# Kernel tuning notes

Hardware: AMD Instinct MI355X
Metric: run time of the kernel (lower is better)

## Reference

```python
import jax, jax.numpy as jnp
import numpy as np

B, S1, T = 32, 128, 50
E, H, L, V = 768, 1024, 3, 32000


def setup_inputs() -> dict:
    key = jax.random.key(0)
    ks = jax.random.split(key, 32)
    s = 0.02
    inp = {
        "x": jax.random.normal(ks[0], (B, S1, E), jnp.float32),
        "target_seq": jax.random.randint(ks[1], (B, T), 0, V),
        "emb": jax.random.normal(ks[2], (V, E), jnp.float32) * s,
        "attn_W1": jax.random.normal(ks[3], (H, E + H), jnp.float32) * s,
        "attn_b1": jnp.zeros((H,), jnp.float32),
        "attn_W2": jax.random.normal(ks[4], (1, H), jnp.float32) * s,
        "attn_b2": jnp.zeros((1,), jnp.float32),
        "fc_W": jax.random.normal(ks[5], (V, H), jnp.float32) * s,
        "fc_b": jnp.zeros((V,), jnp.float32),
    }
    for l in range(L):
        in_dim = 2 * E if l == 0 else H
        inp[f"Wih{l}"] = jax.random.normal(ks[6 + 4 * l], (4 * H, in_dim), jnp.float32) * s
        inp[f"Whh{l}"] = jax.random.normal(ks[7 + 4 * l], (4 * H, H), jnp.float32) * s
        inp[f"bih{l}"] = jnp.zeros((4 * H,), jnp.float32)
        inp[f"bhh{l}"] = jnp.zeros((4 * H,), jnp.float32)
    return inp


def _forward(x, target_seq, emb, attn_W1, attn_b1, attn_W2, attn_b2,
             Wih0, Whh0, bih0, bhh0, Wih1, Whh1, bih1, bhh1,
             Wih2, Whh2, bih2, bhh2, fc_W, fc_b):
    Bb, S, Edim = x.shape
    Hd = Whh0.shape[1]
    W1x, W1h = attn_W1[:, :Edim], attn_W1[:, Edim:]
    # precompute encoder-side part of the additive attention MLP: (B, S, H)
    xW = jnp.einsum('bse,he->bsh', x, W1x)
    emb_in = emb[target_seq]  # teacher forcing inputs (B, T, E)
    Wihs = (Wih0, Wih1, Wih2)
    Whhs = (Whh0, Whh1, Whh2)
    bihs = (bih0, bih1, bih2)
    bhhs = (bhh0, bhh1, bhh2)

    def step(carry, cur_in):
        h, c = carry  # each (L, B, H)
        hid = jax.nn.relu(xW + (h[-1] @ W1h.T)[:, None, :] + attn_b1)  # (B,S,H)
        scores = hid @ attn_W2[0] + attn_b2[0]  # (B, S)
        # NOTE: original module multiplies LOG-softmax weights by x (faithful)
        logw = jax.nn.log_softmax(scores, axis=1)[:, :, None]
        context = jnp.sum(logw * x, axis=1)  # (B, E)
        inp = jnp.concatenate([cur_in, context], axis=1)  # (B, 2E)
        new_h, new_c = [], []
        for l in range(3):
            gates = inp @ Wihs[l].T + h[l] @ Whhs[l].T + bihs[l] + bhhs[l]
            i, f, g, o = jnp.split(gates, 4, axis=1)  # torch gate order i,f,g,o
            cl = jax.nn.sigmoid(f) * c[l] + jax.nn.sigmoid(i) * jnp.tanh(g)
            hl = jax.nn.sigmoid(o) * jnp.tanh(cl)
            new_h.append(hl)
            new_c.append(cl)
            inp = hl
        h = jnp.stack(new_h)
        c = jnp.stack(new_c)
        logits = inp @ fc_W.T + fc_b  # (B, V)
        return (h, c), jax.nn.log_softmax(logits, axis=1)

    h0 = jnp.zeros((3, Bb, Hd), x.dtype)
    c0 = jnp.zeros_like(h0)
    _, outs = jax.lax.scan(step, (h0, c0), jnp.swapaxes(emb_in, 0, 1))
    return jnp.swapaxes(outs, 0, 1)  # (B, T, V)


def reference(x, target_seq, emb, attn_W1, attn_b1, attn_W2, attn_b2,
              Wih0, Whh0, bih0, bhh0, Wih1, Whh1, bih1, bhh1,
              Wih2, Whh2, bih2, bhh2, fc_W, fc_b):
    return _forward(x, target_seq, emb, attn_W1, attn_b1, attn_W2, attn_b2,
                    Wih0, Whh0, bih0, bhh0, Wih1, Whh1, bih1, bhh1,
                    Wih2, Whh2, bih2, bhh2, fc_W, fc_b)
```

## Files before the change

### kernel.cpp

```cpp
#include <hip/hip_runtime.h>
#include <math.h>

#define Bdim 32
#define Sdim 128
#define Tdim 50
#define Edim 768
#define Hdim 1024
#define Vdim 32000
#define EH   1792
#define INPD 1536

typedef __bf16 bf16x8 __attribute__((ext_vector_type(8)));
typedef float  f32x4  __attribute__((ext_vector_type(4)));

__device__ __forceinline__ float sigmf(float v){ return 1.0f / (1.0f + expf(-v)); }

__device__ __forceinline__ ushort f2b(float v){
  unsigned int b = __float_as_uint(v);
  unsigned int r = (b + 0x7fffu + ((b >> 16) & 1u)) >> 16;
  return (ushort)r;
}
__device__ __forceinline__ float b2f(ushort u){
  return __uint_as_float(((unsigned int)u) << 16);
}

__global__ __launch_bounds__(256) void cvt_bf16(const float* __restrict__ src,
                                                ushort* __restrict__ dst, int n4){
  int i = blockIdx.x * 256 + threadIdx.x;
  if (i >= n4) return;
  float4 v = *(const float4*)(src + (size_t)i * 4);
  *(ushort4*)(dst + (size_t)i * 4) = make_ushort4(f2b(v.x), f2b(v.y), f2b(v.z), f2b(v.w));
}

__global__ __launch_bounds__(256) void cvt_w1h(const float* __restrict__ aW1,
                                               ushort* __restrict__ dst){
  int i = blockIdx.x * 256 + threadIdx.x;
  if (i >= 262144) return;
  int k = (i & 255) * 4;
  int j = i >> 8;
  float4 v = *(const float4*)(aW1 + (size_t)j * EH + Edim + k);
  *(ushort4*)(dst + (size_t)j * 1024 + k) = make_ushort4(f2b(v.x), f2b(v.y), f2b(v.z), f2b(v.w));
}

__global__ __launch_bounds__(256) void zero_kernel(float* __restrict__ p, int n){
  int i = blockIdx.x * 256 + threadIdx.x;
  if (i < n) p[i] = 0.0f;
}

__global__ __launch_bounds__(256) void gather_emb_p(const int* __restrict__ tseq,
                                                    const float* __restrict__ emb,
                                                    ushort* __restrict__ inpP){
  int g = blockIdx.x * 256 + threadIdx.x;
  if (g >= Tdim * Bdim * 96) return;
  int kb = g % 96;
  int r = g / 96;
  int b = r % Bdim;
  int t = r / Bdim;
  int tok = tseq[b * Tdim + t];
  const float* src = emb + (size_t)tok * Edim + kb * 8;
  float4 a = *(const float4*)src;
  float4 c = *(const float4*)(src + 4);
  ushort* dst = inpP + (size_t)t * 49152 + kb * 256 + b * 8;
  *(ushort4*)(dst)     = make_ushort4(f2b(a.x), f2b(a.y), f2b(a.z), f2b(a.w));
  *(ushort4*)(dst + 4) = make_ushort4(f2b(c.x), f2b(c.y), f2b(c.z), f2b(c.w));
}

__global__ __launch_bounds__(256) void xw_gemm(const float* __restrict__ x,
                                               const float* __restrict__ w1,
                                               ushort* __restrict__ xWb){
  __shared__ float As[16][68];
  __shared__ float Ws[16][68];
  int tid = threadIdx.x;
  int m0 = blockIdx.x * 64;
  int n0 = blockIdx.y * 64;
  int lm = tid >> 2;
  int lk = (tid & 3) << 2;
  int tm = (tid >> 4) << 2;
  int tn = (tid & 15) << 2;
  float acc[4][4] = {};
  for (int k0 = 0; k0 < Edim; k0 += 16){
    float4 av = *(const float4*)&x [(size_t)(m0 + lm) * Edim + k0 + lk];
    float4 wv = *(const float4*)&w1[(size_t)(n0 + lm) * EH   + k0 + lk];
    As[lk+0][lm] = av.x; As[lk+1][lm] = av.y; As[lk+2][lm] = av.z; As[lk+3][lm] = av.w;
    Ws[lk+0][lm] = wv.x; Ws[lk+1][lm] = wv.y; Ws[lk+2][lm] = wv.z; Ws[lk+3][lm] = wv.w;
    __syncthreads();
#pragma unroll
    for (int k = 0; k < 16; k++){
      float a0 = As[k][tm+0], a1 = As[k][tm+1], a2 = As[k][tm+2], a3 = As[k][tm+3];
      float b0 = Ws[k][tn+0], b1 = Ws[k][tn+1], b2 = Ws[k][tn+2], b3 = Ws[k][tn+3];
      acc[0][0] += a0*b0; acc[0][1] += a0*b1; acc[0][2] += a0*b2; acc[0][3] += a0*b3;
      acc[1][0] += a1*b0; acc[1][1] += a1*b1; acc[1][2] += a1*b2; acc[1][3] += a1*b3;
      acc[2][0] += a2*b0; acc[2][1] += a2*b1; acc[2][2] += a2*b2; acc[2][3] += a2*b3;
      acc[3][0] += a3*b0; acc[3][1] += a3*b1; acc[3][2] += a3*b2; acc[3][3] += a3*b3;
    }
    __syncthreads();
  }
#pragma unroll
  for (int i = 0; i < 4; i++)
#pragma unroll
    for (int j = 0; j < 4; j++)
      xWb[(size_t)(m0 + tm + i) * Hdim + n0 + tn + j] = f2b(acc[i][j]);
}

template<bool ABF16>
__device__ __forceinline__ void mfma_tile(const void* A, int lda, int rowBase,
                                          const ushort* __restrict__ Bp,
                                          int kbeg, int klen, int lane,
                                          f32x4& acc0, f32x4& acc1){
  int r = rowBase + (lane & 15);
  int q = lane >> 4;
  const ushort* Ab = (const ushort*)A;
  const float*  Af = (const float*)A;
#pragma unroll 4
  for (int kk = kbeg; kk < kbeg + klen; kk += 32){
    bf16x8 a;
    if (ABF16){
      a = *reinterpret_cast<const bf16x8*>(Ab + (size_t)r * lda + kk + q * 8);
    } else {
      const float* p = Af + (size_t)r * lda + kk + q * 8;
      float4 u = *(const float4*)p;
      float4 w = *(const float4*)(p + 4);
      union { ushort s[8]; bf16x8 v; } t;
      t.s[0]=f2b(u.x); t.s[1]=f2b(u.y); t.s[2]=f2b(u.z); t.s[3]=f2b(u.w);
      t.s[4]=f2b(w.x); t.s[5]=f2b(w.y); t.s[6]=f2b(w.z); t.s[7]=f2b(w.w);
      a = t.v;
    }
    const ushort* bbase = Bp + ((kk >> 3) + q) * 256 + (lane & 15) * 8;
    bf16x8 b0 = *reinterpret_cast<const bf16x8*>(bbase);
    bf16x8 b1 = *reinterpret_cast<const bf16x8*>(bbase + 128);
    acc0 = __builtin_amdgcn_mfma_f32_16x16x32_bf16(a, b0, acc0, 0, 0, 0);
    acc1 = __builtin_amdgcn_mfma_f32_16x16x32_bf16(a, b1, acc1, 0, 0, 0);
  }
}

template<bool ABF16>
__global__ __launch_bounds__(256) void gate_gemm(const void* __restrict__ Wih, int Kin,
                                                 const void* __restrict__ Whh,
                                                 const ushort* __restrict__ inpP,
                                                 const ushort* __restrict__ hP,
                                                 float* __restrict__ part){
  int lane = threadIdx.x & 63, w = threadIdx.x >> 6;
  int rowBase = blockIdx.x * 64 + w * 16;
  int kq = blockIdx.y;
  f32x4 acc0 = {0,0,0,0}, acc1 = {0,0,0,0};
  if (kq < 2) mfma_tile<ABF16>(Wih, Kin, rowBase, inpP, kq * (Kin >> 1), Kin >> 1, lane, acc0, acc1);
  else        mfma_tile<ABF16>(Whh, Hdim, rowBase, hP, (kq - 2) * 512, 512, lane, acc0, acc1);
  float* dst = part + (size_t)kq * (4096 * 32);
  int q = lane >> 4, c = lane & 15;
#pragma unroll
  for (int rr = 0; rr < 4; rr++){
    int row = rowBase + q * 4 + rr;
    dst[row * 32 + c]      = acc0[rr];
    dst[row * 32 + 16 + c] = acc1[rr];
  }
}

__global__ __launch_bounds__(256) void cell_update(const float* __restrict__ part,
                                                   const float* __restrict__ bih,
                                                   const float* __restrict__ bhh,
                                                   const float* __restrict__ cold,
                                                   float* __restrict__ cnew,
                                                   ushort* __restrict__ hPack){
  int idx = blockIdx.x * 256 + threadIdx.x;
  int b = idx & 31, j = idx >> 5;
  float gi = 0, gf = 0, gg = 0, go = 0;
#pragma unroll
  for (int kq = 0; kq < 4; kq++){
    const float* p = part + (size_t)kq * 131072;
    gi += p[j * 32 + b];
    gf += p[(j + 1024) * 32 + b];
    gg += p[(j + 2048) * 32 + b];
    go += p[(j + 3072) * 32 + b];
  }
  gi += bih[j]        + bhh[j];
  gf += bih[j + 1024] + bhh[j + 1024];
  gg += bih[j + 2048] + bhh[j + 2048];
  go += bih[j + 3072] + bhh[j + 3072];
  float cv = sigmf(gf) * cold[j * 32 + b] + sigmf(gi) * tanhf(gg);
  float hv = sigmf(go) * tanhf(cv);
  cnew[j * 32 + b] = cv;
  hPack[(j >> 3) * 256 + b * 8 + (j & 7)] = f2b(hv);
}

__global__ __launch_bounds__(256) void attn_a_gemm(const ushort* __restrict__ W1h,
                                                   const ushort* __restrict__ h2P,
                                                   float* __restrict__ part){
  int lane = threadIdx.x & 63, w = threadIdx.x >> 6;
  int rowBase = blockIdx.x * 64 + w * 16;
  int kq = blockIdx.y;
  f32x4 acc0 = {0,0,0,0}, acc1 = {0,0,0,0};
  mfma_tile<true>(W1h, Hdim, rowBase, h2P, kq * 256, 256, lane, acc0, acc1);
  float* dst = part + (size_t)kq * 32768;
  int q = lane >> 4, c = lane & 15;
#pragma unroll
  for (int rr = 0; rr < 4; rr++){
    int row = rowBase + q * 4 + rr;
    dst[c * 1024 + row]        = acc0[rr];
    dst[(c + 16) * 1024 + row] = acc1[rr];
  }
}

__global__ __launch_bounds__(256) void attn_score(const float* __restrict__ aPart,
                                                  const float* __restrict__ b1,
                                                  const float* __restrict__ w2,
                                                  const float* __restrict__ b2p,
                                                  const ushort* __restrict__ xWb,
                                                  float* __restrict__ scBuf){
  int b = blockIdx.x >> 2, sg = blockIdx.x & 3;
  int w = threadIdx.x >> 6, lane = threadIdx.x & 63;
  float ab[16], wv[16];
#pragma unroll
  for (int i = 0; i < 16; i++){
    int j = lane + 64 * i;
    float av = aPart[b * 1024 + j] + aPart[32768 + b * 1024 + j]
             + aPart[65536 + b * 1024 + j] + aPart[98304 + b * 1024 + j];
    ab[i] = av + b1[j];
    wv[i] = w2[j];
  }
  float b2v = b2p[0];
#pragma unroll
  for (int si = 0; si < 8; si++){
    int s = sg * 32 + w * 8 + si;
    const ushort* xrow = xWb + (size_t)(b * Sdim + s) * Hdim;
    float acc = 0.0f;
#pragma unroll
    for (int i = 0; i < 16; i++){
      float xv = b2f(xrow[lane + 64 * i]);
      float hv = fmaxf(xv + ab[i], 0.0f);
      acc += hv * wv[i];
    }
    for (int off = 32; off; off >>= 1) acc += __shfl_xor(acc, off);
    if (lane == 0) scBuf[b * Sdim + s] = acc + b2v;
  }
}

__global__ __launch_bounds__(256) void attn_ctx2(const float* __restrict__ scBuf,
                                                 const float* __restrict__ x,
                                                 ushort* __restrict__ inpPt){
  __shared__ float sb[Sdim];
  __shared__ float lseS;
  int b = blockIdx.x / 3, ec = blockIdx.x % 3;
  int tid = threadIdx.x;
  if (tid < Sdim) sb[tid] = scBuf[b * Sdim + tid];
  __syncthreads();
  if (tid < 64){
    float v0 = sb[tid], v1 = sb[tid + 64];
    float m = fmaxf(v0, v1);
    for (int off = 32; off; off >>= 1) m = fmaxf(m, __shfl_xor(m, off));
    float e = expf(v0 - m) + expf(v1 - m);
    for (int off = 32; off; off >>= 1) e += __shfl_xor(e, off);
    if (tid == 0) lseS = m + logf(e);
  }
  __syncthreads();
  float lse = lseS;
  int e = ec * 256 + tid;
  const float* xb = x + (size_t)b * Sdim * Edim + e;
  float acc = 0.0f;
#pragma unroll 8
  for (int s = 0; s < Sdim; s++) acc += (sb[s] - lse) * xb[(size_t)s * Edim];
  int k = Edim + e;
  inpPt[(k >> 3) * 256 + b * 8 + (k & 7)] = f2b(acc);
}

template<bool ABF16>
__global__ __launch_bounds__(256) void fc_gemm(const void* __restrict__ fcW,
                                               const ushort* __restrict__ hP,
                                               const float* __restrict__ fcb,
                                               float* __restrict__ logits){
  __shared__ float ld[32][65];
  int lane = threadIdx.x & 63, w = threadIdx.x >> 6;
  int v0 = blockIdx.x * 64 + w * 16;
  f32x4 acc0 = {0,0,0,0}, acc1 = {0,0,0,0};
  mfma_tile<ABF16>(fcW, Hdim, v0, hP, 0, Hdim, lane, acc0, acc1);
  int q = lane >> 4, c = lane & 15;
#pragma unroll
  for (int rr = 0; rr < 4; rr++){
    int vloc = w * 16 + q * 4 + rr;
    ld[c][vloc]      = acc0[rr];
    ld[c + 16][vloc] = acc1[rr];
  }
  __syncthreads();
  int b = threadIdx.x >> 3, i8 = (threadIdx.x & 7) * 8;
  int vg = blockIdx.x * 64 + i8;
  float4 o0, o1;
  o0.x = ld[b][i8+0] + fcb[vg+0]; o0.y = ld[b][i8+1] + fcb[vg+1];
  o0.z = ld[b][i8+2] + fcb[vg+2]; o0.w = ld[b][i8+3] + fcb[vg+3];
  o1.x = ld[b][i8+4] + fcb[vg+4]; o1.y = ld[b][i8+5] + fcb[vg+5];
  o1.z = ld[b][i8+6] + fcb[vg+6]; o1.w = ld[b][i8+7] + fcb[vg+7];
  *(float4*)&logits[(size_t)b * Vdim + vg]     = o0;
  *(float4*)&logits[(size_t)b * Vdim + vg + 4] = o1;
}

__global__ __launch_bounds__(1024) void lsm_reduce(const float* __restrict__ logits,
                                                   float* __restrict__ lse){
  __shared__ float red[1024];
  int b = blockIdx.x, tid = threadIdx.x;
  const float4* row4 = (const float4*)(logits + (size_t)b * Vdim);
  float m = -1e30f;
  for (int i = tid; i < Vdim / 4; i += 1024){
    float4 v = row4[i];
    m = fmaxf(m, fmaxf(fmaxf(v.x, v.y), fmaxf(v.z, v.w)));
  }
  red[tid] = m; __syncthreads();
  for (int s = 512; s; s >>= 1){
    if (tid < s) red[tid] = fmaxf(red[tid], red[tid + s]);
    __syncthreads();
  }
  m = red[0]; __syncthreads();
  float sum = 0.0f;
  for (int i = tid; i < Vdim / 4; i += 1024){
    float4 v = row4[i];
    sum += expf(v.x - m) + expf(v.y - m) + expf(v.z - m) + expf(v.w - m);
  }
  red[tid] = sum; __syncthreads();
  for (int s = 512; s; s >>= 1){
    if (tid < s) red[tid] += red[tid + s];
    __syncthreads();
  }
  if (tid == 0) lse[b] = m + logf(red[0]);
}

__global__ __launch_bounds__(256) void lsm_write(const float* __restrict__ logits,
                                                 const float* __restrict__ lse,
                                                 float* __restrict__ out, int t){
  int i = blockIdx.x * 256 + threadIdx.x;
  if (i >= Bdim * Vdim / 4) return;
  int b = i / (Vdim / 4);
  float l = lse[b];
  float4 v = ((const float4*)logits)[i];
  float4* dst = (float4*)(out + ((size_t)b * Tdim + t) * Vdim);
  dst[i - b * (Vdim / 4)] = make_float4(v.x - l, v.y - l, v.z - l, v.w - l);
}

extern "C" void kernel_launch(void* const* d_in, const int* in_sizes, int n_in,
                              void* d_out, int out_size, void* d_ws, size_t ws_size,
                              hipStream_t stream){
  const float* x    = (const float*)d_in[0];
  const int*   tseq = (const int*)  d_in[1];
  const float* emb  = (const float*)d_in[2];
  const float* aW1  = (const float*)d_in[3];
  const float* ab1  = (const float*)d_in[4];
  const float* aW2  = (const float*)d_in[5];
  const float* ab2  = (const float*)d_in[6];
  const float* fcW  = (const float*)d_in[7];
  const float* fcb  = (const float*)d_in[8];
  const float* Wih[3] = {(const float*)d_in[9],  (const float*)d_in[13], (const float*)d_in[17]};
  const float* Whh[3] = {(const float*)d_in[10], (const float*)d_in[14], (const float*)d_in[18]};
  const float* bih[3] = {(const float*)d_in[11], (const float*)d_in[15], (const float*)d_in[19]};
  const float* bhh[3] = {(const float*)d_in[12], (const float*)d_in[16], (const float*)d_in[20]};
  float* out = (float*)d_out;

  char* p = (char*)d_ws;
  ushort* xW_bf  = (ushort*)p;            p += (size_t)4096 * 1024 * 2;
  ushort* W1h_bf = (ushort*)p;            p += (size_t)1024 * 1024 * 2;
  ushort* inpP   = (ushort*)p;            p += (size_t)Tdim * 49152 * 2;
  float*  aPart  = (float*)p;             p += (size_t)4 * 32768 * 4;
  float*  scBuf  = (float*)p;             p += (size_t)Bdim * Sdim * 4;
  float*  lseBuf = (float*)p;             p += 256;
  float*  gPart  = (float*)p;             p += (size_t)4 * 131072 * 4;
  float*  logits = (float*)p;             p += (size_t)Bdim * Vdim * 4;
  float*  cBuf   = (float*)p;             p += (size_t)6 * 32768 * 4;
  ushort* hPackB = (ushort*)p;            p += (size_t)6 * 32768 * 2;
  ushort* fcW_bf  = (ushort*)p;           p += (size_t)Vdim * Hdim * 2;
  ushort* Wih_bf[3]; ushort* Whh_bf[3];
  Wih_bf[0] = (ushort*)p;                 p += (size_t)4096 * 1536 * 2;
  Whh_bf[0] = (ushort*)p;                 p += (size_t)4096 * 1024 * 2;
  Wih_bf[1] = (ushort*)p;                 p += (size_t)4096 * 1024 * 2;
  Whh_bf[1] = (ushort*)p;                 p += (size_t)4096 * 1024 * 2;
  Wih_bf[2] = (ushort*)p;                 p += (size_t)4096 * 1024 * 2;
  Whh_bf[2] = (ushort*)p;                 p += (size_t)4096 * 1024 * 2;
  size_t need_full = (size_t)(p - (char*)d_ws);
  bool full = ws_size >= need_full;

  zero_kernel<<<(294912 + 255) / 256, 256, 0, stream>>>(cBuf, 294912);
  gather_emb_p<<<(Tdim * Bdim * 96 + 255) / 256, 256, 0, stream>>>(tseq, emb, inpP);
  cvt_w1h<<<262144 / 256, 256, 0, stream>>>(aW1, W1h_bf);
  xw_gemm<<<dim3(64, 16), 256, 0, stream>>>(x, aW1, xW_bf);
  if (full){
    cvt_bf16<<<(Vdim * Hdim / 4 + 255) / 256, 256, 0, stream>>>(fcW, fcW_bf, Vdim * Hdim / 4);
    cvt_bf16<<<(4096 * 1536 / 4 + 255) / 256, 256, 0, stream>>>(Wih[0], Wih_bf[0], 4096 * 1536 / 4);
    cvt_bf16<<<(4096 * 1024 / 4 + 255) / 256, 256, 0, stream>>>(Whh[0], Whh_bf[0], 4096 * 1024 / 4);
    cvt_bf16<<<(4096 * 1024 / 4 + 255) / 256, 256, 0, stream>>>(Wih[1], Wih_bf[1], 4096 * 1024 / 4);
    cvt_bf16<<<(4096 * 1024 / 4 + 255) / 256, 256, 0, stream>>>(Whh[1], Whh_bf[1], 4096 * 1024 / 4);
    cvt_bf16<<<(4096 * 1024 / 4 + 255) / 256, 256, 0, stream>>>(Wih[2], Wih_bf[2], 4096 * 1024 / 4);
    cvt_bf16<<<(4096 * 1024 / 4 + 255) / 256, 256, 0, stream>>>(Whh[2], Whh_bf[2], 4096 * 1024 / 4);
  }

  #define HP(l, par)  (hPackB + ((l) * 2 + (par)) * 32768)
  #define CB(l, par)  (cBuf   + ((l) * 2 + (par)) * 32768)

  for (int t = 0; t < Tdim; t++){
    int pn = t & 1, po = 1 - pn;
    ushort* inpPt = inpP + (size_t)t * 49152;

    attn_a_gemm<<<dim3(16, 4), 256, 0, stream>>>(W1h_bf, HP(2, po), aPart);
    attn_score<<<128, 256, 0, stream>>>(aPart, ab1, aW2, ab2, xW_bf, scBuf);
    attn_ctx2<<<96, 256, 0, stream>>>(scBuf, x, inpPt);

    for (int l = 0; l < 3; l++){
      const ushort* bin = (l == 0) ? inpPt : HP(l - 1, pn);
      int kin = (l == 0) ? INPD : Hdim;
      if (full)
        gate_gemm<true ><<<dim3(64, 4), 256, 0, stream>>>(Wih_bf[l], kin, Whh_bf[l], bin, HP(l, po), gPart);
      else
        gate_gemm<false><<<dim3(64, 4), 256, 0, stream>>>(Wih[l],    kin, Whh[l],    bin, HP(l, po), gPart);
      cell_update<<<128, 256, 0, stream>>>(gPart, bih[l], bhh[l], CB(l, po), CB(l, pn), HP(l, pn));
    }

    if (full) fc_gemm<true ><<<Vdim / 64, 256, 0, stream>>>(fcW_bf, HP(2, pn), fcb, logits);
    else      fc_gemm<false><<<Vdim / 64, 256, 0, stream>>>(fcW,    HP(2, pn), fcb, logits);
    lsm_reduce<<<Bdim, 1024, 0, stream>>>(logits, lseBuf);
    lsm_write<<<(Bdim * Vdim / 4 + 255) / 256, 256, 0, stream>>>(logits, lseBuf, out, t);
  }
}
```

Measured before the change: 4.855 ms.

## Fuse LSTM gate GEMM with cell update and fold softmax stats into FC GEMM

Merges the gate GEMM and cell-update kernels into one 512-thread kernel that reduces split-K partials in shared memory, which removes the global partial buffer and one launch per layer. It also computes per-block online max/sum-exp inside the FC GEMM, so a small finalize kernel replaces the two-pass logits reduction. It vectorizes xW loads in the attention score, and converts x to bf16 once for the context sum. This cuts launches and memory traffic per step, at the cost of bf16 precision in the context sum and fewer blocks in the LSTM layer (64 blocks).

```diff
diff --git a/kernel.cpp b/kernel.cpp
--- a/kernel.cpp
+++ b/kernel.cpp
@@ -9,6 +9,7 @@
 #define Vdim 32000
 #define EH   1792
 #define INPD 1536
+#define FCB  500
 
 typedef __bf16 bf16x8 __attribute__((ext_vector_type(8)));
 typedef float  f32x4  __attribute__((ext_vector_type(4)));
@@ -134,48 +135,40 @@
 }
 
 template<bool ABF16>
-__global__ __launch_bounds__(256) void gate_gemm(const void* __restrict__ Wih, int Kin,
-                                                 const void* __restrict__ Whh,
-                                                 const ushort* __restrict__ inpP,
-                                                 const ushort* __restrict__ hP,
-                                                 float* __restrict__ part){
-  int lane = threadIdx.x & 63, w = threadIdx.x >> 6;
-  int rowBase = blockIdx.x * 64 + w * 16;
-  int kq = blockIdx.y;
+__global__ __launch_bounds__(512) void lstm_layer(const void* __restrict__ Wih, int Kin,
+                                                  const void* __restrict__ Whh,
+                                                  const ushort* __restrict__ inpP,
+                                                  const ushort* __restrict__ hP,
+                                                  const float* __restrict__ bih,
+                                                  const float* __restrict__ bhh,
+                                                  const float* __restrict__ cold,
+                                                  float* __restrict__ cnew,
+                                                  ushort* __restrict__ hPack){
+  __shared__ float ld[8][32][18];
+  int tid = threadIdx.x;
+  int lane = tid & 63, w = tid >> 6;
+  int gate = w & 3, khalf = w >> 2;
+  int j0 = blockIdx.x * 16;
+  int rowBase = gate * 1024 + j0;
   f32x4 acc0 = {0,0,0,0}, acc1 = {0,0,0,0};
-  if (kq < 2) mfma_tile<ABF16>(Wih, Kin, rowBase, inpP, kq * (Kin >> 1), Kin >> 1, lane, acc0, acc1);
-  else        mfma_tile<ABF16>(Whh, Hdim, rowBase, hP, (kq - 2) * 512, 512, lane, acc0, acc1);
-  float* dst = part + (size_t)kq * (4096 * 32);
+  int kin_half = Kin >> 1;
+  size_t wih_row = ABF16 ? (size_t)Kin : (size_t)Kin;
+  mfma_tile<ABF16>(Wih, Kin, rowBase, inpP, khalf * kin_half, kin_half, lane, acc0, acc1);
+  mfma_tile<ABF16>(Whh, Hdim, rowBase, hP, khalf * 512, 512, lane, acc0, acc1);
+  (void)wih_row;
   int q = lane >> 4, c = lane & 15;
 #pragma unroll
   for (int rr = 0; rr < 4; rr++){
-    int row = rowBase + q * 4 + rr;
-    dst[row * 32 + c]      = acc0[rr];
-    dst[row * 32 + 16 + c] = acc1[rr];
-  }
-}
-
-__global__ __launch_bounds__(256) void cell_update(const float* __restrict__ part,
-                                                   const float* __restrict__ bih,
-                                                   const float* __restrict__ bhh,
-                                                   const float* __restrict__ cold,
-                                                   float* __restrict__ cnew,
-                                                   ushort* __restrict__ hPack){
-  int idx = blockIdx.x * 256 + threadIdx.x;
-  int b = idx & 31, j = idx >> 5;
-  float gi = 0, gf = 0, gg = 0, go = 0;
-#pragma unroll
-  for (int kq = 0; kq < 4; kq++){
-    const float* p = part + (size_t)kq * 131072;
-    gi += p[j * 32 + b];
-    gf += p[(j + 1024) * 32 + b];
-    gg += p[(j + 2048) * 32 + b];
-    go += p[(j + 3072) * 32 + b];
-  }
-  gi += bih[j]        + bhh[j];
-  gf += bih[j + 1024] + bhh[j + 1024];
-  gg += bih[j + 2048] + bhh[j + 2048];
-  go += bih[j + 3072] + bhh[j + 3072];
+    ld[w][c][q * 4 + rr]      = acc0[rr];
+    ld[w][c + 16][q * 4 + rr] = acc1[rr];
+  }
+  __syncthreads();
+  int b = tid & 31, jl = tid >> 5;
+  int j = j0 + jl;
+  float gi = ld[0][b][jl] + ld[4][b][jl] + bih[j]        + bhh[j];
+  float gf = ld[1][b][jl] + ld[5][b][jl] + bih[j + 1024] + bhh[j + 1024];
+  float gg = ld[2][b][jl] + ld[6][b][jl] + bih[j + 2048] + bhh[j + 2048];
+  float go = ld[3][b][jl] + ld[7][b][jl] + bih[j + 3072] + bhh[j + 3072];
   float cv = sigmf(gf) * cold[j * 32 + b] + sigmf(gi) * tanhf(gg);
   float hv = sigmf(go) * tanhf(cv);
   cnew[j * 32 + b] = cv;
@@ -208,10 +201,11 @@
                                                   float* __restrict__ scBuf){
   int b = blockIdx.x >> 2, sg = blockIdx.x & 3;
   int w = threadIdx.x >> 6, lane = threadIdx.x & 63;
+  int jb = lane * 16;
   float ab[16], wv[16];
 #pragma unroll
   for (int i = 0; i < 16; i++){
-    int j = lane + 64 * i;
+    int j = jb + i;
     float av = aPart[b * 1024 + j] + aPart[32768 + b * 1024 + j]
              + aPart[65536 + b * 1024 + j] + aPart[98304 + b * 1024 + j];
     ab[i] = av + b1[j];
@@ -221,13 +215,15 @@
 #pragma unroll
   for (int si = 0; si < 8; si++){
     int s = sg * 32 + w * 8 + si;
-    const ushort* xrow = xWb + (size_t)(b * Sdim + s) * Hdim;
+    const ushort* xrow = xWb + (size_t)(b * Sdim + s) * Hdim + jb;
+    bf16x8 x0 = *reinterpret_cast<const bf16x8*>(xrow);
+    bf16x8 x1 = *reinterpret_cast<const bf16x8*>(xrow + 8);
     float acc = 0.0f;
 #pragma unroll
-    for (int i = 0; i < 16; i++){
-      float xv = b2f(xrow[lane + 64 * i]);
-      float hv = fmaxf(xv + ab[i], 0.0f);
-      acc += hv * wv[i];
+    for (int i = 0; i < 8; i++){
+      float h0 = fmaxf((float)x0[i] + ab[i], 0.0f);
+      float h1 = fmaxf((float)x1[i] + ab[i + 8], 0.0f);
+      acc += h0 * wv[i] + h1 * wv[i + 8];
     }
     for (int off = 32; off; off >>= 1) acc += __shfl_xor(acc, off);
     if (lane == 0) scBuf[b * Sdim + s] = acc + b2v;
@@ -235,10 +231,9 @@
 }
 
 __global__ __launch_bounds__(256) void attn_ctx2(const float* __restrict__ scBuf,
-                                                 const float* __restrict__ x,
+                                                 const ushort* __restrict__ xbf,
                                                  ushort* __restrict__ inpPt){
   __shared__ float sb[Sdim];
-  __shared__ float lseS;
   int b = blockIdx.x / 3, ec = blockIdx.x % 3;
   int tid = threadIdx.x;
   if (tid < Sdim) sb[tid] = scBuf[b * Sdim + tid];
@@ -249,75 +244,90 @@
     for (int off = 32; off; off >>= 1) m = fmaxf(m, __shfl_xor(m, off));
     float e = expf(v0 - m) + expf(v1 - m);
     for (int off = 32; off; off >>= 1) e += __shfl_xor(e, off);
-    if (tid == 0) lseS = m + logf(e);
+    float lse = m + logf(e);
+    sb[tid]      = v0 - lse;
+    sb[tid + 64] = v1 - lse;
   }
   __syncthreads();
-  float lse = lseS;
   int e = ec * 256 + tid;
-  const float* xb = x + (size_t)b * Sdim * Edim + e;
+  const ushort* xb = xbf + (size_t)b * Sdim * Edim + e;
   float acc = 0.0f;
 #pragma unroll 8
-  for (int s = 0; s < Sdim; s++) acc += (sb[s] - lse) * xb[(size_t)s * Edim];
+  for (int s = 0; s < Sdim; s++) acc += sb[s] * b2f(xb[(size_t)s * Edim]);
   int k = Edim + e;
   inpPt[(k >> 3) * 256 + b * 8 + (k & 7)] = f2b(acc);
 }
 
 template<bool ABF16>
-__global__ __launch_bounds__(256) void fc_gemm(const void* __restrict__ fcW,
+__global__ __launch_bounds__(512) void fc_gemm(const void* __restrict__ fcW,
                                                const ushort* __restrict__ hP,
                                                const float* __restrict__ fcb,
-                                               float* __restrict__ logits){
-  __shared__ float ld[32][65];
-  int lane = threadIdx.x & 63, w = threadIdx.x >> 6;
-  int v0 = blockIdx.x * 64 + w * 16;
+                                               float* __restrict__ logits,
+                                               float* __restrict__ partM,
+                                               float* __restrict__ partS){
+  __shared__ float ld[2][32][72];
+  int tid = threadIdx.x;
+  int lane = tid & 63, w = tid >> 6;
+  int khalf = w >> 2;
+  int v0 = blockIdx.x * 64 + (w & 3) * 16;
   f32x4 acc0 = {0,0,0,0}, acc1 = {0,0,0,0};
-  mfma_tile<ABF16>(fcW, Hdim, v0, hP, 0, Hdim, lane, acc0, acc1);
+  mfma_tile<ABF16>(fcW, Hdim, v0, hP, khalf * 512, 512, lane, acc0, acc1);
   int q = lane >> 4, c = lane & 15;
 #pragma unroll
   for (int rr = 0; rr < 4; rr++){
-    int vloc = w * 16 + q * 4 + rr;
-    ld[c][vloc]      = acc0[rr];
-    ld[c + 16][vloc] = acc1[rr];
+    int vloc = (w & 3) * 16 + q * 4 + rr;
+    ld[khalf][c][vloc]      = acc0[rr];
+    ld[khalf][c + 16][vloc] = acc1[rr];
   }
   __syncthreads();
-  int b = threadIdx.x >> 3, i8 = (threadIdx.x & 7) * 8;
-  int vg = blockIdx.x * 64 + i8;
-  float4 o0, o1;
-  o0.x = ld[b][i8+0] + fcb[vg+0]; o0.y = ld[b][i8+1] + fcb[vg+1];
-  o0.z = ld[b][i8+2] + fcb[vg+2]; o0.w = ld[b][i8+3] + fcb[vg+3];
-  o1.x = ld[b][i8+4] + fcb[vg+4]; o1.y = ld[b][i8+5] + fcb[vg+5];
-  o1.z = ld[b][i8+6] + fcb[vg+6]; o1.w = ld[b][i8+7] + fcb[vg+7];
-  *(float4*)&logits[(size_t)b * Vdim + vg]     = o0;
-  *(float4*)&logits[(size_t)b * Vdim + vg + 4] = o1;
-}
-
-__global__ __launch_bounds__(1024) void lsm_reduce(const float* __restrict__ logits,
-                                                   float* __restrict__ lse){
-  __shared__ float red[1024];
+  int b = tid >> 4, i0 = (tid & 15) * 4;
+  int vg = blockIdx.x * 64 + i0;
+  float o0 = ld[0][b][i0+0] + ld[1][b][i0+0] + fcb[vg+0];
+  float o1 = ld[0][b][i0+1] + ld[1][b][i0+1] + fcb[vg+1];
+  float o2 = ld[0][b][i0+2] + ld[1][b][i0+2] + fcb[vg+2];
+  float o3 = ld[0][b][i0+3] + ld[1][b][i0+3] + fcb[vg+3];
+  *(float4*)&logits[(size_t)b * Vdim + vg] = make_float4(o0, o1, o2, o3);
+  float m = fmaxf(fmaxf(o0, o1), fmaxf(o2, o3));
+  float s = expf(o0 - m) + expf(o1 - m) + expf(o2 - m) + expf(o3 - m);
+#pragma unroll
+  for (int off = 1; off < 16; off <<= 1){
+    float m2 = __shfl_xor(m, off);
+    float s2 = __shfl_xor(s, off);
+    float nm = fmaxf(m, m2);
+    s = s * expf(m - nm) + s2 * expf(m2 - nm);
+    m = nm;
+  }
+  if ((tid & 15) == 0){
+    partM[b * FCB + blockIdx.x] = m;
+    partS[b * FCB + blockIdx.x] = s;
+  }
+}
+
+__global__ __launch_bounds__(256) void lsm_finalize(const float* __restrict__ partM,
+                                                    const float* __restrict__ partS,
+                                                    float* __restrict__ lse){
+  __shared__ float sm[256], ss[256];
   int b = blockIdx.x, tid = threadIdx.x;
-  const float4* row4 = (const float4*)(logits + (size_t)b * Vdim);
-  float m = -1e30f;
-  for (int i = tid; i < Vdim / 4; i += 1024){
-    float4 v = row4[i];
-    m = fmaxf(m, fmaxf(fmaxf(v.x, v.y), fmaxf(v.z, v.w)));
-  }
-  red[tid] = m; __syncthreads();
-  for (int s = 512; s; s >>= 1){
-    if (tid < s) red[tid] = fmaxf(red[tid], red[tid + s]);
+  float m = -1e30f, s = 0.0f;
+  for (int i = tid; i < FCB; i += 256){
+    float m2 = partM[b * FCB + i];
+    float s2 = partS[b * FCB + i];
+    float nm = fmaxf(m, m2);
+    s = s * expf(m - nm) + s2 * expf(m2 - nm);
+    m = nm;
+  }
+  sm[tid] = m; ss[tid] = s;
+  __syncthreads();
+  for (int r = 128; r; r >>= 1){
+    if (tid < r){
+      float m2 = sm[tid + r], s2 = ss[tid + r];
+      float nm = fmaxf(sm[tid], m2);
+      ss[tid] = ss[tid] * expf(sm[tid] - nm) + s2 * expf(m2 - nm);
+      sm[tid] = nm;
+    }
     __syncthreads();
   }
-  m = red[0]; __syncthreads();
-  float sum = 0.0f;
-  for (int i = tid; i < Vdim / 4; i += 1024){
-    float4 v = row4[i];
-    sum += expf(v.x - m) + expf(v.y - m) + expf(v.z - m) + expf(v.w - m);
-  }
-  red[tid] = sum; __syncthreads();
-  for (int s = 512; s; s >>= 1){
-    if (tid < s) red[tid] += red[tid + s];
-    __syncthreads();
-  }
-  if (tid == 0) lse[b] = m + logf(red[0]);
+  if (tid == 0) lse[b] = sm[0] + logf(ss[0]);
 }
 
 __global__ __launch_bounds__(256) void lsm_write(const float* __restrict__ logits,
@@ -354,10 +364,12 @@
   ushort* xW_bf  = (ushort*)p;            p += (size_t)4096 * 1024 * 2;
   ushort* W1h_bf = (ushort*)p;            p += (size_t)1024 * 1024 * 2;
   ushort* inpP   = (ushort*)p;            p += (size_t)Tdim * 49152 * 2;
+  ushort* x_bf   = (ushort*)p;            p += (size_t)Bdim * Sdim * Edim * 2;
   float*  aPart  = (float*)p;             p += (size_t)4 * 32768 * 4;
   float*  scBuf  = (float*)p;             p += (size_t)Bdim * Sdim * 4;
   float*  lseBuf = (float*)p;             p += 256;
-  float*  gPart  = (float*)p;             p += (size_t)4 * 131072 * 4;
+  float*  partM  = (float*)p;             p += (size_t)Bdim * FCB * 4;
+  float*  partS  = (float*)p;             p += (size_t)Bdim * FCB * 4;
   float*  logits = (float*)p;             p += (size_t)Bdim * Vdim * 4;
   float*  cBuf   = (float*)p;             p += (size_t)6 * 32768 * 4;
   ushort* hPackB = (ushort*)p;            p += (size_t)6 * 32768 * 2;
@@ -375,6 +387,7 @@
   zero_kernel<<<(294912 + 255) / 256, 256, 0, stream>>>(cBuf, 294912);
   gather_emb_p<<<(Tdim * Bdim * 96 + 255) / 256, 256, 0, stream>>>(tseq, emb, inpP);
   cvt_w1h<<<262144 / 256, 256, 0, stream>>>(aW1, W1h_bf);
+  cvt_bf16<<<(Bdim * Sdim * Edim / 4 + 255) / 256, 256, 0, stream>>>(x, x_bf, Bdim * Sdim * Edim / 4);
   xw_gemm<<<dim3(64, 16), 256, 0, stream>>>(x, aW1, xW_bf);
   if (full){
     cvt_bf16<<<(Vdim * Hdim / 4 + 255) / 256, 256, 0, stream>>>(fcW, fcW_bf, Vdim * Hdim / 4);
@@ -395,21 +408,22 @@
 
     attn_a_gemm<<<dim3(16, 4), 256, 0, stream>>>(W1h_bf, HP(2, po), aPart);
     attn_score<<<128, 256, 0, stream>>>(aPart, ab1, aW2, ab2, xW_bf, scBuf);
-    attn_ctx2<<<96, 256, 0, stream>>>(scBuf, x, inpPt);
+    attn_ctx2<<<96, 256, 0, stream>>>(scBuf, x_bf, inpPt);
 
     for (int l = 0; l < 3; l++){
       const ushort* bin = (l == 0) ? inpPt : HP(l - 1, pn);
       int kin = (l == 0) ? INPD : Hdim;
       if (full)
-        gate_gemm<true ><<<dim3(64, 4), 256, 0, stream>>>(Wih_bf[l], kin, Whh_bf[l], bin, HP(l, po), gPart);
+        lstm_layer<true ><<<64, 512, 0, stream>>>(Wih_bf[l], kin, Whh_bf[l], bin, HP(l, po),
+                                                  bih[l], bhh[l], CB(l, po), CB(l, pn), HP(l, pn));
       else
-        gate_gemm<false><<<dim3(64, 4), 256, 0, stream>>>(Wih[l],    kin, Whh[l],    bin, HP(l, po), gPart);
-      cell_update<<<128, 256, 0, stream>>>(gPart, bih[l], bhh[l], CB(l, po), CB(l, pn), HP(l, pn));
+        lstm_layer<false><<<64, 512, 0, stream>>>(Wih[l],    kin, Whh[l],    bin, HP(l, po),
+                                                  bih[l], bhh[l], CB(l, po), CB(l, pn), HP(l, pn));
     }
 
-    if (full) fc_gemm<true ><<<Vdim / 64, 256, 0, stream>>>(fcW_bf, HP(2, pn), fcb, logits);
-    else      fc_gemm<false><<<Vdim / 64, 256, 0, stream>>>(fcW,    HP(2, pn), fcb, logits);
-    lsm_reduce<<<Bdim, 1024, 0, stream>>>(logits, lseBuf);
+    if (full) fc_gemm<true ><<<FCB, 512, 0, stream>>>(fcW_bf, HP(2, pn), fcb, logits, partM, partS);
+    else      fc_gemm<false><<<FCB, 512, 0, stream>>>(fcW,    HP(2, pn), fcb, logits, partM, partS);
+    lsm_finalize<<<Bdim, 256, 0, stream>>>(partM, partS, lseBuf);
     lsm_write<<<(Bdim * Vdim / 4 + 255) / 256, 256, 0, stream>>>(logits, lseBuf, out, t);
   }
 }
```

New measurement: 5.312 ms. 9.4% more time.
